# Optimization experiments

Measured on AMD Instinct MI355X. Metric: run time of the kernel, lower is better.

Reference implementation:

```python
import jax, jax.numpy as jnp
import numpy as np

DIM, HEADS = 512, 8
HD = DIM // HEADS
B, T = 1, 512


def _rope_tables(T, hd):
    inv_freq = 1.0 / (10000.0 ** (jnp.arange(0, hd, 2, dtype=jnp.float32) / hd))
    freqs = jnp.arange(T, dtype=jnp.float32)[:, None] * inv_freq[None, :]
    emb = jnp.concatenate([freqs, freqs], axis=-1)  # [T, hd]
    return jnp.cos(emb), jnp.sin(emb)


def _rotate_half_heads(x):
    # Faithful to source: torch chunk(2, dim=1) on [B,H,hd,1,T] splits the HEADS axis.
    x1, x2 = jnp.split(x, 2, axis=1)
    return jnp.concatenate([-x2, x1], axis=1)


def setup_inputs():
    key = jax.random.key(0)
    ks = jax.random.split(key, 5)
    s = 1.0 / np.sqrt(DIM)
    return {
        "x": jax.random.normal(ks[0], (B, T, DIM), dtype=jnp.float32),
        "Wq": jax.random.normal(ks[1], (DIM, DIM), dtype=jnp.float32) * s,
        "Wk": jax.random.normal(ks[2], (DIM, DIM), dtype=jnp.float32) * s,
        "Wv": jax.random.normal(ks[3], (DIM, DIM), dtype=jnp.float32) * s,
        "Wo": jax.random.normal(ks[4], (DIM, DIM), dtype=jnp.float32) * s,
    }


def reference(x, Wq, Wk, Wv, Wo):
    b, t, d = x.shape
    h, hd = HEADS, d // HEADS
    scale = 1.0 / np.sqrt(hd)

    def proj(W):
        # 1x1 Conv2d == per-position linear; channel o = head*hd + c  -> [B,H,hd,T]
        return jnp.einsum('btd,od->bot', x, W).reshape(b, h, hd, t)

    q, k, v = proj(Wq), proj(Wk), proj(Wv)

    cos, sin = _rope_tables(t, hd)
    cosT = cos.T[None, None]  # [1,1,hd,T]
    sinT = sin.T[None, None]
    q = q * cosT + _rotate_half_heads(q) * sinT
    k = k * cosT + _rotate_half_heads(k) * sinT

    # Per-channel outer-product scores (inner dim of the matmul is the singleton axis)
    att = jnp.einsum('bhci,bhcj->bhcij', q, k) * scale  # [B,H,hd,T,T]
    causal_mask = jnp.triu(jnp.ones((t, t), dtype=bool), k=1)
    att = jnp.where(causal_mask, -jnp.inf, att)
    att = jax.nn.softmax(att, axis=-1)

    out = jnp.einsum('bhcij,bhcj->bhci', att, v).reshape(b, d, t)
    return jnp.einsum('od,bdt->bto', Wo, out)  # [B,T,D]
```

## Files before the change

kernel.cpp:

```cpp
#include <hip/hip_runtime.h>
#include <math.h>

typedef __attribute__((ext_vector_type(8))) short short8;
typedef __attribute__((ext_vector_type(4))) float floatx4;

__device__ __forceinline__ unsigned short f2bf(float f) {
    unsigned int u = __builtin_bit_cast(unsigned int, f);
    u += 0x7FFFu + ((u >> 16) & 1u);
    return (unsigned short)(u >> 16);
}


__global__ __launch_bounds__(256) void cvt_bf16(
    const float* __restrict__ x,  const float* __restrict__ Wq,
    const float* __restrict__ Wk, const float* __restrict__ Wv,
    const float* __restrict__ Wo, unsigned short* __restrict__ Wallb,
    unsigned short* __restrict__ xb, unsigned short* __restrict__ Wob)
{
    const float* src; unsigned short* dst;
    switch (blockIdx.y) {
        case 0: src = Wq; dst = Wallb;          break;
        case 1: src = Wk; dst = Wallb + 262144; break;
        case 2: src = Wv; dst = Wallb + 524288; break;
        case 3: src = x;  dst = xb;             break;
        default: src = Wo; dst = Wob;           break;
    }
    const int i4 = (blockIdx.x * 256 + threadIdx.x) * 4;
    const float4 v = *(const float4*)(src + i4);
    ushort4 o;
    o.x = f2bf(v.x); o.y = f2bf(v.y); o.z = f2bf(v.z); o.w = f2bf(v.w);
    *(ushort4*)(dst + i4) = o;
}

__global__ __launch_bounds__(256) void gemm_bt(
    const unsigned short* __restrict__ A,
    const unsigned short* __restrict__ B,
    float* __restrict__ C)
{
    __shared__ unsigned short As[64 * 64];
    __shared__ unsigned short Bs[64 * 64];

    const int tid  = threadIdx.x;
    const int lane = tid & 63;
    const int w    = tid >> 6;
    const int m0   = blockIdx.y * 64;
    const int n0   = blockIdx.x * 64;
    const int wm   = (w >> 1) * 32;
    const int wn   = (w & 1) * 32;

    const int srow8 = w * 8 + (lane >> 3);
    const int c8    = lane & 7;

    floatx4 acc[2][2] = {{{0.f,0.f,0.f,0.f},{0.f,0.f,0.f,0.f}},
                         {{0.f,0.f,0.f,0.f},{0.f,0.f,0.f,0.f}}};

    const int quad = lane >> 4;
    const int l15  = lane & 15;

    for (int kc = 0; kc < 512; kc += 64) {
        #pragma unroll
        for (int rr = 0; rr < 2; ++rr) {
            const int row  = rr * 32 + srow8;
            const int gcol = kc + ((c8 ^ (row & 7)) * 8);
            const unsigned short* ga = A + (m0 + row) * 512 + gcol;
            const unsigned short* gb = B + (n0 + row) * 512 + gcol;
            __builtin_amdgcn_global_load_lds(
                (const __attribute__((address_space(1))) void*)ga,
                (__attribute__((address_space(3))) void*)&As[(rr * 32 + w * 8) * 64],
                16, 0, 0);
            __builtin_amdgcn_global_load_lds(
                (const __attribute__((address_space(1))) void*)gb,
                (__attribute__((address_space(3))) void*)&Bs[(rr * 32 + w * 8) * 64],
                16, 0, 0);
        }
        __syncthreads();

        #pragma unroll
        for (int ks = 0; ks < 2; ++ks) {
            const int cIdx = ks * 4 + quad;
            short8 a[2], b[2];
            #pragma unroll
            for (int mt = 0; mt < 2; ++mt) {
                const int row = wm + mt * 16 + l15;
                a[mt] = *(const short8*)&As[row * 64 + ((cIdx ^ (row & 7)) * 8)];
            }
            #pragma unroll
            for (int nt = 0; nt < 2; ++nt) {
                const int row = wn + nt * 16 + l15;
                b[nt] = *(const short8*)&Bs[row * 64 + ((cIdx ^ (row & 7)) * 8)];
            }
            #pragma unroll
            for (int mt = 0; mt < 2; ++mt)
                #pragma unroll
                for (int nt = 0; nt < 2; ++nt)
                    acc[mt][nt] = __builtin_amdgcn_mfma_f32_16x16x32_bf16(
                        a[mt], b[nt], acc[mt][nt], 0, 0, 0);
        }
        __syncthreads();
    }

    #pragma unroll
    for (int mt = 0; mt < 2; ++mt)
        #pragma unroll
        for (int nt = 0; nt < 2; ++nt) {
            const int grow = m0 + wm + mt * 16 + quad * 4;
            const int gcol = n0 + wn + nt * 16 + l15;
            #pragma unroll
            for (int r = 0; r < 4; ++r)
                C[(grow + r) * 512 + gcol] = acc[mt][nt][r];
        }
}

__global__ __launch_bounds__(512) void attn_rope(
    const float* __restrict__ qkv, float* __restrict__ att)
{
    const int ch = blockIdx.x;
    const int i  = threadIdx.x;
    const int c  = ch & 63;
    const int p  = ch ^ 256;
    const float sgn = (ch < 256) ? -1.f : 1.f;

    __shared__ float ks_[512];
    __shared__ float vs_[512];

    const float* __restrict__ qg = qkv;
    const float* __restrict__ kg = qkv + 262144;
    const float* __restrict__ vg = qkv + 524288;

    const float inv_freq = powf(10000.f, -(float)(c & 31) * (1.f / 32.f));
    float sn, cs;
    sincosf((float)i * inv_freq, &sn, &cs);

    const float kv = kg[ch * 512 + i], kpv = kg[p * 512 + i];
    ks_[i] = (kv * cs + sgn * kpv * sn) * 0.125f;
    vs_[i] = vg[ch * 512 + i];
    const float qv = qg[ch * 512 + i], qpv = qg[p * 512 + i];
    const float qi = qv * cs + sgn * qpv * sn;
    __syncthreads();

    float l = 0.f, acc = 0.f;
    const int jend = i & ~63;

    #pragma unroll 2
    for (int j = 0; j < jend; j += 4) {
        const float4 a4 = *(const float4*)&ks_[j];
        const float4 v4 = *(const float4*)&vs_[j];
        float e;
        e = __expf(qi * a4.x); l += e; acc = fmaf(e, v4.x, acc);
        e = __expf(qi * a4.y); l += e; acc = fmaf(e, v4.y, acc);
        e = __expf(qi * a4.z); l += e; acc = fmaf(e, v4.z, acc);
        e = __expf(qi * a4.w); l += e; acc = fmaf(e, v4.w, acc);
    }
    #pragma unroll
    for (int u = 0; u < 64; u += 4) {
        const int j = jend + u;
        const float4 a4 = *(const float4*)&ks_[j];
        const float4 v4 = *(const float4*)&vs_[j];
        float e;
        e = (j + 0 <= i) ? __expf(qi * a4.x) : 0.f; l += e; acc = fmaf(e, v4.x, acc);
        e = (j + 1 <= i) ? __expf(qi * a4.y) : 0.f; l += e; acc = fmaf(e, v4.y, acc);
        e = (j + 2 <= i) ? __expf(qi * a4.z) : 0.f; l += e; acc = fmaf(e, v4.z, acc);
        e = (j + 3 <= i) ? __expf(qi * a4.w) : 0.f; l += e; acc = fmaf(e, v4.w, acc);
    }
    att[ch * 512 + i] = acc / l;
}

__global__ __launch_bounds__(256) void attT_cvt(
    const float* __restrict__ att, unsigned short* __restrict__ attTb)
{
    __shared__ float tile[32][33];
    const int d0 = blockIdx.y * 32, t0 = blockIdx.x * 32;
    const int tx = threadIdx.x, ty = threadIdx.y;
    #pragma unroll
    for (int i = 0; i < 32; i += 8)
        tile[ty + i][tx] = att[(d0 + ty + i) * 512 + t0 + tx];
    __syncthreads();
    #pragma unroll
    for (int i = 0; i < 32; i += 8)
        attTb[(t0 + ty + i) * 512 + d0 + tx] = f2bf(tile[tx][ty + i]);
}

extern "C" void kernel_launch(void* const* d_in, const int* in_sizes, int n_in,
                              void* d_out, int out_size, void* d_ws, size_t ws_size,
                              hipStream_t stream)
{
    const float* x  = (const float*)d_in[0];
    const float* Wq = (const float*)d_in[1];
    const float* Wk = (const float*)d_in[2];
    const float* Wv = (const float*)d_in[3];
    const float* Wo = (const float*)d_in[4];
    float* out = (float*)d_out;

    unsigned short* Wallb = (unsigned short*)d_ws;
    unsigned short* xb    = Wallb + 786432;
    unsigned short* Wob   = xb + 262144;
    unsigned short* attTb = Wob + 262144;
    float* qkvf = (float*)(attTb + 262144);
    float* attf = qkvf + 786432;

    cvt_bf16<<<dim3(256, 5), 256, 0, stream>>>(x, Wq, Wk, Wv, Wo, Wallb, xb, Wob);
    gemm_bt<<<dim3(8, 24), 256, 0, stream>>>(Wallb, xb, qkvf);
    attn_rope<<<512, 512, 0, stream>>>(qkvf, attf);
    attT_cvt<<<dim3(16, 16), dim3(32, 8), 0, stream>>>(attf, attTb);
    gemm_bt<<<dim3(8, 8), 256, 0, stream>>>(attTb, Wob, out);
}
```

Before: 102.6 us.

## Fuse attention output transpose into attention kernel and use LDS-free wave GEMMs

Replaces the LDS-tiled 256-thread GEMM with a single-wave GEMM that loads bf16 fragments directly from global memory into MFMA operands. Rewrites the per-channel attention so each 128-thread block processes four query rows per thread, with sin/cos tables computed once in shared memory. The attention result is written transposed as bf16 directly, removing the separate transpose/convert kernel and the fp32 intermediate buffer. In exchange, the transposed store is strided and there is less thread-level parallelism per channel.

```diff
diff --git a/kernel.cpp b/kernel.cpp
--- a/kernel.cpp
+++ b/kernel.cpp
@@ -32,152 +32,124 @@
     *(ushort4*)(dst + i4) = o;
 }
 
-__global__ __launch_bounds__(256) void gemm_bt(
-    const unsigned short* __restrict__ A,
-    const unsigned short* __restrict__ B,
+__global__ __launch_bounds__(64) void gemm_wave(
+    const unsigned short* __restrict__ A, const unsigned short* __restrict__ B,
     float* __restrict__ C)
 {
-    __shared__ unsigned short As[64 * 64];
-    __shared__ unsigned short Bs[64 * 64];
-
-    const int tid  = threadIdx.x;
-    const int lane = tid & 63;
-    const int w    = tid >> 6;
-    const int m0   = blockIdx.y * 64;
-    const int n0   = blockIdx.x * 64;
-    const int wm   = (w >> 1) * 32;
-    const int wn   = (w & 1) * 32;
-
-    const int srow8 = w * 8 + (lane >> 3);
-    const int c8    = lane & 7;
+    const int lane = threadIdx.x;
+    const int quad = lane >> 4, l15 = lane & 15;
+    const int m0 = (blockIdx.x >> 4) * 32;
+    const int n0 = (blockIdx.x & 15) * 32;
 
     floatx4 acc[2][2] = {{{0.f,0.f,0.f,0.f},{0.f,0.f,0.f,0.f}},
                          {{0.f,0.f,0.f,0.f},{0.f,0.f,0.f,0.f}}};
 
-    const int quad = lane >> 4;
-    const int l15  = lane & 15;
+    const unsigned short* a0 = A + (m0 + l15) * 512 + quad * 8;
+    const unsigned short* a1 = a0 + 16 * 512;
+    const unsigned short* b0 = B + (n0 + l15) * 512 + quad * 8;
+    const unsigned short* b1 = b0 + 16 * 512;
 
-    for (int kc = 0; kc < 512; kc += 64) {
-        #pragma unroll
-        for (int rr = 0; rr < 2; ++rr) {
-            const int row  = rr * 32 + srow8;
-            const int gcol = kc + ((c8 ^ (row & 7)) * 8);
-            const unsigned short* ga = A + (m0 + row) * 512 + gcol;
-            const unsigned short* gb = B + (n0 + row) * 512 + gcol;
-            __builtin_amdgcn_global_load_lds(
-                (const __attribute__((address_space(1))) void*)ga,
-                (__attribute__((address_space(3))) void*)&As[(rr * 32 + w * 8) * 64],
-                16, 0, 0);
-            __builtin_amdgcn_global_load_lds(
-                (const __attribute__((address_space(1))) void*)gb,
-                (__attribute__((address_space(3))) void*)&Bs[(rr * 32 + w * 8) * 64],
-                16, 0, 0);
-        }
-        __syncthreads();
-
-        #pragma unroll
-        for (int ks = 0; ks < 2; ++ks) {
-            const int cIdx = ks * 4 + quad;
-            short8 a[2], b[2];
-            #pragma unroll
-            for (int mt = 0; mt < 2; ++mt) {
-                const int row = wm + mt * 16 + l15;
-                a[mt] = *(const short8*)&As[row * 64 + ((cIdx ^ (row & 7)) * 8)];
-            }
-            #pragma unroll
-            for (int nt = 0; nt < 2; ++nt) {
-                const int row = wn + nt * 16 + l15;
-                b[nt] = *(const short8*)&Bs[row * 64 + ((cIdx ^ (row & 7)) * 8)];
-            }
-            #pragma unroll
-            for (int mt = 0; mt < 2; ++mt)
-                #pragma unroll
-                for (int nt = 0; nt < 2; ++nt)
-                    acc[mt][nt] = __builtin_amdgcn_mfma_f32_16x16x32_bf16(
-                        a[mt], b[nt], acc[mt][nt], 0, 0, 0);
-        }
-        __syncthreads();
+    #pragma unroll 4
+    for (int kc = 0; kc < 512; kc += 32) {
+        const short8 av0 = *(const short8*)(a0 + kc);
+        const short8 av1 = *(const short8*)(a1 + kc);
+        const short8 bv0 = *(const short8*)(b0 + kc);
+        const short8 bv1 = *(const short8*)(b1 + kc);
+        acc[0][0] = __builtin_amdgcn_mfma_f32_16x16x32_bf16(av0, bv0, acc[0][0], 0, 0, 0);
+        acc[0][1] = __builtin_amdgcn_mfma_f32_16x16x32_bf16(av0, bv1, acc[0][1], 0, 0, 0);
+        acc[1][0] = __builtin_amdgcn_mfma_f32_16x16x32_bf16(av1, bv0, acc[1][0], 0, 0, 0);
+        acc[1][1] = __builtin_amdgcn_mfma_f32_16x16x32_bf16(av1, bv1, acc[1][1], 0, 0, 0);
     }
 
     #pragma unroll
     for (int mt = 0; mt < 2; ++mt)
         #pragma unroll
         for (int nt = 0; nt < 2; ++nt) {
-            const int grow = m0 + wm + mt * 16 + quad * 4;
-            const int gcol = n0 + wn + nt * 16 + l15;
+            const int grow = m0 + mt * 16 + quad * 4;
+            const int gcol = n0 + nt * 16 + l15;
             #pragma unroll
             for (int r = 0; r < 4; ++r)
                 C[(grow + r) * 512 + gcol] = acc[mt][nt][r];
         }
 }
 
-__global__ __launch_bounds__(512) void attn_rope(
-    const float* __restrict__ qkv, float* __restrict__ att)
+__global__ __launch_bounds__(128) void attn_rope4(
+    const float* __restrict__ qkv, unsigned short* __restrict__ attTb)
 {
-    const int ch = blockIdx.x;
-    const int i  = threadIdx.x;
-    const int c  = ch & 63;
-    const int p  = ch ^ 256;
+    const int ch   = blockIdx.x;
+    const int tid  = threadIdx.x;
+    const int w    = tid >> 6;
+    const int lane = tid & 63;
+    const int p    = ch ^ 256;
     const float sgn = (ch < 256) ? -1.f : 1.f;
 
     __shared__ float ks_[512];
     __shared__ float vs_[512];
+    __shared__ float cs_[512];
+    __shared__ float sn_[512];
 
     const float* __restrict__ qg = qkv;
     const float* __restrict__ kg = qkv + 262144;
     const float* __restrict__ vg = qkv + 524288;
 
-    const float inv_freq = powf(10000.f, -(float)(c & 31) * (1.f / 32.f));
-    float sn, cs;
-    sincosf((float)i * inv_freq, &sn, &cs);
+    const float inv_freq = powf(10000.f, -(float)(ch & 31) * (1.f / 32.f));
 
-    const float kv = kg[ch * 512 + i], kpv = kg[p * 512 + i];
-    ks_[i] = (kv * cs + sgn * kpv * sn) * 0.125f;
-    vs_[i] = vg[ch * 512 + i];
-    const float qv = qg[ch * 512 + i], qpv = qg[p * 512 + i];
-    const float qi = qv * cs + sgn * qpv * sn;
+    {
+        const int t0 = tid * 4;
+        const float4 kc4 = *(const float4*)(kg + ch * 512 + t0);
+        const float4 kp4 = *(const float4*)(kg + p  * 512 + t0);
+        const float4 vv4 = *(const float4*)(vg + ch * 512 + t0);
+        const float kc_[4] = {kc4.x, kc4.y, kc4.z, kc4.w};
+        const float kp_[4] = {kp4.x, kp4.y, kp4.z, kp4.w};
+        const float vv_[4] = {vv4.x, vv4.y, vv4.z, vv4.w};
+        #pragma unroll
+        for (int u = 0; u < 4; ++u) {
+            float sn, cs;
+            sincosf((float)(t0 + u) * inv_freq, &sn, &cs);
+            ks_[t0 + u] = (kc_[u] * cs + sgn * kp_[u] * sn) * 0.125f;
+            vs_[t0 + u] = vv_[u];
+            cs_[t0 + u] = cs;
+            sn_[t0 + u] = sn;
+        }
+    }
     __syncthreads();
 
-    float l = 0.f, acc = 0.f;
-    const int jend = i & ~63;
+    float qi[4], l[4] = {0.f, 0.f, 0.f, 0.f}, acc[4] = {0.f, 0.f, 0.f, 0.f};
+    #pragma unroll
+    for (int r = 0; r < 4; ++r) {
+        const int i = r * 128 + tid;
+        qi[r] = qg[ch * 512 + i] * cs_[i] + sgn * qg[p * 512 + i] * sn_[i];
+    }
 
-    #pragma unroll 2
-    for (int j = 0; j < jend; j += 4) {
-        const float4 a4 = *(const float4*)&ks_[j];
-        const float4 v4 = *(const float4*)&vs_[j];
-        float e;
-        e = __expf(qi * a4.x); l += e; acc = fmaf(e, v4.x, acc);
-        e = __expf(qi * a4.y); l += e; acc = fmaf(e, v4.y, acc);
-        e = __expf(qi * a4.z); l += e; acc = fmaf(e, v4.z, acc);
-        e = __expf(qi * a4.w); l += e; acc = fmaf(e, v4.w, acc);
+    const int Bmax = 6 + w;
+    for (int B = 0; B <= Bmax; ++B) {
+        const int bm = B - w;
+        for (int jj = 0; jj < 64; jj += 4) {
+            const float4 k4 = *(const float4*)&ks_[B * 64 + jj];
+            const float4 v4 = *(const float4*)&vs_[B * 64 + jj];
+            #pragma unroll
+            for (int r = 0; r < 4; ++r) {
+                if (bm > 2 * r) continue;
+                if (bm < 2 * r) {
+                    float e;
+                    e = __expf(qi[r] * k4.x); l[r] += e; acc[r] = fmaf(e, v4.x, acc[r]);
+                    e = __expf(qi[r] * k4.y); l[r] += e; acc[r] = fmaf(e, v4.y, acc[r]);
+                    e = __expf(qi[r] * k4.z); l[r] += e; acc[r] = fmaf(e, v4.z, acc[r]);
+                    e = __expf(qi[r] * k4.w); l[r] += e; acc[r] = fmaf(e, v4.w, acc[r]);
+                } else {
+                    float e;
+                    e = (jj + 0 <= lane) ? __expf(qi[r] * k4.x) : 0.f; l[r] += e; acc[r] = fmaf(e, v4.x, acc[r]);
+                    e = (jj + 1 <= lane) ? __expf(qi[r] * k4.y) : 0.f; l[r] += e; acc[r] = fmaf(e, v4.y, acc[r]);
+                    e = (jj + 2 <= lane) ? __expf(qi[r] * k4.z) : 0.f; l[r] += e; acc[r] = fmaf(e, v4.z, acc[r]);
+                    e = (jj + 3 <= lane) ? __expf(qi[r] * k4.w) : 0.f; l[r] += e; acc[r] = fmaf(e, v4.w, acc[r]);
+                }
+            }
+        }
     }
+
     #pragma unroll
-    for (int u = 0; u < 64; u += 4) {
-        const int j = jend + u;
-        const float4 a4 = *(const float4*)&ks_[j];
-        const float4 v4 = *(const float4*)&vs_[j];
-        float e;
-        e = (j + 0 <= i) ? __expf(qi * a4.x) : 0.f; l += e; acc = fmaf(e, v4.x, acc);
-        e = (j + 1 <= i) ? __expf(qi * a4.y) : 0.f; l += e; acc = fmaf(e, v4.y, acc);
-        e = (j + 2 <= i) ? __expf(qi * a4.z) : 0.f; l += e; acc = fmaf(e, v4.z, acc);
-        e = (j + 3 <= i) ? __expf(qi * a4.w) : 0.f; l += e; acc = fmaf(e, v4.w, acc);
-    }
-    att[ch * 512 + i] = acc / l;
-}
-
-__global__ __launch_bounds__(256) void attT_cvt(
-    const float* __restrict__ att, unsigned short* __restrict__ attTb)
-{
-    __shared__ float tile[32][33];
-    const int d0 = blockIdx.y * 32, t0 = blockIdx.x * 32;
-    const int tx = threadIdx.x, ty = threadIdx.y;
-    #pragma unroll
-    for (int i = 0; i < 32; i += 8)
-        tile[ty + i][tx] = att[(d0 + ty + i) * 512 + t0 + tx];
-    __syncthreads();
-    #pragma unroll
-    for (int i = 0; i < 32; i += 8)
-        attTb[(t0 + ty + i) * 512 + d0 + tx] = f2bf(tile[tx][ty + i]);
+    for (int r = 0; r < 4; ++r)
+        attTb[(r * 128 + tid) * 512 + ch] = f2bf(acc[r] / l[r]);
 }
 
 extern "C" void kernel_launch(void* const* d_in, const int* in_sizes, int n_in,
@@ -196,11 +168,9 @@
     unsigned short* Wob   = xb + 262144;
     unsigned short* attTb = Wob + 262144;
     float* qkvf = (float*)(attTb + 262144);
-    float* attf = qkvf + 786432;
 
     cvt_bf16<<<dim3(256, 5), 256, 0, stream>>>(x, Wq, Wk, Wv, Wo, Wallb, xb, Wob);
-    gemm_bt<<<dim3(8, 24), 256, 0, stream>>>(Wallb, xb, qkvf);
-    attn_rope<<<512, 512, 0, stream>>>(qkvf, attf);
-    attT_cvt<<<dim3(16, 16), dim3(32, 8), 0, stream>>>(attf, attTb);
-    gemm_bt<<<dim3(8, 8), 256, 0, stream>>>(attTb, Wob, out);
+    gemm_wave<<<768, 64, 0, stream>>>(Wallb, xb, qkvf);
+    attn_rope4<<<512, 128, 0, stream>>>(qkvf, attTb);
+    gemm_wave<<<256, 64, 0, stream>>>(attTb, Wob, out);
 }
```

Result: slower. 122.2 us (+19.1%).
